# Kernel optimization log

Measured on AMD Instinct MI355X. Metric: run time of the kernel, lower is better.

## Reference

```python
import jax, jax.numpy as jnp
import numpy as np

N_NODES = 50000
IN, HID, OUT = 128, 128, 47
N_EDGES = 800000


def _glorot(key, shape):
    fan_in, fan_out = shape[1], shape[0]
    lim = np.sqrt(6.0 / (fan_in + fan_out)).astype(np.float32)
    return jax.random.uniform(key, shape, jnp.float32, -lim, lim)


def setup_inputs() -> dict:
    key = jax.random.key(0)
    ks = jax.random.split(key, 12)
    x = jax.random.normal(ks[0], (N_NODES, IN), jnp.float32)
    src = jax.random.randint(ks[1], (N_EDGES,), 0, N_NODES)
    dst = jax.random.randint(ks[2], (N_EDGES,), 0, N_NODES)
    return {
        "x": x, "src": src, "dst": dst,
        "w_self1": _glorot(ks[3], (HID, IN)),  "w_neigh1": _glorot(ks[4], (HID, IN)),  "b1": jnp.zeros((HID,), jnp.float32),
        "w_self2": _glorot(ks[5], (HID, HID)), "w_neigh2": _glorot(ks[6], (HID, HID)), "b2": jnp.zeros((HID,), jnp.float32),
        "w_self3": _glorot(ks[7], (OUT, HID)), "w_neigh3": _glorot(ks[8], (OUT, HID)), "b3": jnp.zeros((OUT,), jnp.float32),
    }


def _sage_conv(h, src, dst, w_self, w_neigh, b):
    # gather src features, mean-reduce per dst node (DGL copy_u + mean)
    msg = h[src]                                                  # [E, d]
    agg = jax.ops.segment_sum(msg, dst, num_segments=N_NODES)    # [N, d]
    deg = jax.ops.segment_sum(jnp.ones((dst.shape[0],), h.dtype), dst, num_segments=N_NODES)
    mean = agg / jnp.maximum(deg, 1.0)[:, None]
    # DGL SAGEConv('mean'): fc_self(h_dst) + fc_neigh(h_neigh); bias on fc_self only
    return h @ w_self.T + b + mean @ w_neigh.T


def reference(x, src, dst,
              w_self1, w_neigh1, b1,
              w_self2, w_neigh2, b2,
              w_self3, w_neigh3, b3):
    h = _sage_conv(x, src, dst, w_self1, w_neigh1, b1)
    h = jax.nn.relu(h)  # dropout is identity in eval mode
    h = _sage_conv(h, src, dst, w_self2, w_neigh2, b2)
    h = jax.nn.relu(h)
    h = _sage_conv(h, src, dst, w_self3, w_neigh3, b3)
    return h
```

## Files before the change

### kernel.cpp

```cpp
#include <hip/hip_runtime.h>

#define N_NODES 50000
#define N_EDGES 800000
#define DIM 128
#define OUTD 47
#define NBK 196
#define EPB 4096
#define NBIN ((N_EDGES + EPB - 1) / EPB)
#define XCVT_NB (N_NODES * DIM / 8 / 256)
#define WFNB 19

typedef __attribute__((ext_vector_type(8))) short v8s;
typedef __attribute__((ext_vector_type(8))) unsigned short v8u;
typedef __attribute__((ext_vector_type(4))) float v4f;
typedef __attribute__((ext_vector_type(2))) float v2f;

static __device__ __forceinline__ unsigned short f2bf(float f) {
    union { float f; unsigned int u; } v; v.f = f;
    unsigned int x = v.u;
    return (unsigned short)((x + 0x7fffu + ((x >> 16) & 1u)) >> 16);
}
static __device__ __forceinline__ unsigned char f2fp8(float f) {
    unsigned int pk = __builtin_amdgcn_cvt_pk_fp8_f32(f, f, 0, false);
    return (unsigned char)(pk & 0xffu);
}

__global__ __launch_bounds__(256) void k_prep(const float* __restrict__ x,
                                              unsigned short* __restrict__ xb,
                                              unsigned int* __restrict__ x8,
                                              const int* __restrict__ dst,
                                              int* __restrict__ parts,
                                              const float* __restrict__ ws1, const float* __restrict__ wn1,
                                              const float* __restrict__ ws2, const float* __restrict__ wn2,
                                              const float* __restrict__ ws3, const float* __restrict__ wn3,
                                              unsigned short* __restrict__ wf1,
                                              unsigned short* __restrict__ wf2,
                                              unsigned short* __restrict__ wf3) {
    __shared__ int hist[NBK];
    const int bx = blockIdx.x, tid = threadIdx.x;
    if (bx < XCVT_NB) {
        int i = bx * 256 + tid;
        float4 v0 = ((const float4*)x)[i * 2];
        float4 v1 = ((const float4*)x)[i * 2 + 1];
        ushort4 o0, o1;
        o0.x = f2bf(v0.x); o0.y = f2bf(v0.y); o0.z = f2bf(v0.z); o0.w = f2bf(v0.w);
        o1.x = f2bf(v1.x); o1.y = f2bf(v1.y); o1.z = f2bf(v1.z); o1.w = f2bf(v1.w);
        ((ushort4*)xb)[i * 2] = o0;
        ((ushort4*)xb)[i * 2 + 1] = o1;
        unsigned int a = __builtin_amdgcn_cvt_pk_fp8_f32(v0.x, v0.y, 0, false);
        a = __builtin_amdgcn_cvt_pk_fp8_f32(v0.z, v0.w, a, true);
        unsigned int b = __builtin_amdgcn_cvt_pk_fp8_f32(v1.x, v1.y, 0, false);
        b = __builtin_amdgcn_cvt_pk_fp8_f32(v1.z, v1.w, b, true);
        uint2 o; o.x = a; o.y = b;
        ((uint2*)x8)[i] = o;
    } else if (bx < XCVT_NB + NBIN) {
        const int j = bx - XCVT_NB;
        for (int i = tid; i < NBK; i += 256) hist[i] = 0;
        __syncthreads();
        const int e0 = j * EPB;
        const int ecnt = min(EPB, N_EDGES - e0);
        for (int r = tid; r < ecnt; r += 256)
            atomicAdd(&hist[dst[e0 + r] >> 8], 1);
        __syncthreads();
        for (int i = tid; i < NBK; i += 256) parts[j * NBK + i] = hist[i];
    } else {
        int b2 = bx - XCVT_NB - NBIN;
        const float *sw, *nw; unsigned short* ob; int t, J;
        if (b2 < 8)       { sw = ws1; nw = wn1; ob = wf1; t = b2;      J = DIM; }
        else if (b2 < 16) { sw = ws2; nw = wn2; ob = wf2; t = b2 - 8;  J = DIM; }
        else              { sw = ws3; nw = wn3; ob = wf3; t = b2 - 16; J = OUTD; }
        const int lane = tid & 63, cp = tid >> 6;
        const int j = t * 16 + (lane & 15);
        const int kb = (lane >> 4) * 8;
        #pragma unroll
        for (int c2 = 0; c2 < 2; ++c2) {
            int c = cp * 2 + c2;
            int k0 = c * 32 + kb;
            v8u o;
            #pragma unroll
            for (int i = 0; i < 8; ++i) {
                int k = k0 + i;
                float v = 0.f;
                if (j < J) v = (k < DIM) ? sw[j * DIM + k] : nw[j * DIM + (k - DIM)];
                o[i] = f2bf(v);
            }
            *(v8u*)(ob + ((size_t)((t * 8 + c) * 64 + lane)) * 8) = o;
        }
    }
}

__global__ __launch_bounds__(256) void k_bin(const int* __restrict__ src,
                                             const int* __restrict__ dst,
                                             const int* __restrict__ parts,
                                             unsigned int* __restrict__ packed) {
    __shared__ int s[256], gb[NBK], cnt[NBK];
    const int t = threadIdx.x;
    const int j = blockIdx.x;
    int ct = 0, cp = 0;
    for (int i = 0; i < NBIN; ++i) {
        int v = (t < NBK) ? parts[i * NBK + t] : 0;
        if (i == j) cp = ct;
        ct += v;
    }
    s[t] = ct;
    __syncthreads();
    for (int off = 1; off < 256; off <<= 1) {
        int u = (t >= off) ? s[t - off] : 0;
        __syncthreads();
        s[t] += u;
        __syncthreads();
    }
    if (t < NBK) { gb[t] = (s[t] - ct) + cp; cnt[t] = 0; }
    __syncthreads();
    const int e0 = j * EPB;
    const int ecnt = min(EPB, N_EDGES - e0);
    for (int r = t; r < ecnt; r += 256) {
        int sv = src[e0 + r], d = dst[e0 + r];
        int b = d >> 8;
        int loc = atomicAdd(&cnt[b], 1);
        packed[gb[b] + loc] = ((unsigned int)sv << 8) | (unsigned int)(d & 255);
    }
}

__global__ __launch_bounds__(256) void k_place(const unsigned int* __restrict__ packed,
                                               const int* __restrict__ parts,
                                               int* __restrict__ row_ptr,
                                               int* __restrict__ src_sorted) {
    __shared__ int s[256], baseL[NBK], totL[NBK];
    __shared__ int hist[256], cur[256];
    const int b = blockIdx.x, t = threadIdx.x;
    int ct = 0;
    for (int i = 0; i < NBIN; ++i)
        ct += (t < NBK) ? parts[i * NBK + t] : 0;
    s[t] = ct;
    hist[t] = 0;
    __syncthreads();
    for (int off = 1; off < 256; off <<= 1) {
        int u = (t >= off) ? s[t - off] : 0;
        __syncthreads();
        s[t] += u;
        __syncthreads();
    }
    if (t < NBK) { baseL[t] = s[t] - ct; totL[t] = ct; }
    __syncthreads();
    const int base = baseL[b], cb = totL[b];
    for (int i = t; i < cb; i += 256)
        atomicAdd(&hist[packed[base + i] & 255u], 1);
    __syncthreads();
    int v = hist[t];
    s[t] = v;
    __syncthreads();
    for (int off = 1; off < 256; off <<= 1) {
        int u = (t >= off) ? s[t - off] : 0;
        __syncthreads();
        s[t] += u;
        __syncthreads();
    }
    int excl = base + s[t] - v;
    int node = b * 256 + t;
    if (node < N_NODES) row_ptr[node] = excl;
    if (b == NBK - 1 && t == 255) row_ptr[N_NODES] = base + cb;
    cur[t] = excl;
    __syncthreads();
    for (int i = t; i < cb; i += 256) {
        unsigned int pkt = packed[base + i];
        int pos = atomicAdd(&cur[pkt & 255u], 1);
        src_sorted[pos] = (int)(pkt >> 8);
    }
}

static __device__ __forceinline__ void acc16(v2f* acc, uint4 u) {
    acc[0] += __builtin_amdgcn_cvt_pk_f32_fp8(u.x, false);
    acc[1] += __builtin_amdgcn_cvt_pk_f32_fp8(u.x, true);
    acc[2] += __builtin_amdgcn_cvt_pk_f32_fp8(u.y, false);
    acc[3] += __builtin_amdgcn_cvt_pk_f32_fp8(u.y, true);
    acc[4] += __builtin_amdgcn_cvt_pk_f32_fp8(u.z, false);
    acc[5] += __builtin_amdgcn_cvt_pk_f32_fp8(u.z, true);
    acc[6] += __builtin_amdgcn_cvt_pk_f32_fp8(u.w, false);
    acc[7] += __builtin_amdgcn_cvt_pk_f32_fp8(u.w, true);
}

template <int NT, bool RELU, bool OUTBF>
__global__ __launch_bounds__(256, 4) void k_layer(const unsigned short* __restrict__ Ab,
                                                  const unsigned char* __restrict__ g8,
                                                  const int* __restrict__ row_ptr,
                                                  const int* __restrict__ srcs,
                                                  const unsigned short* __restrict__ Wf,
                                                  const float* __restrict__ bias,
                                                  void* __restrict__ out,
                                                  unsigned char* __restrict__ out8,
                                                  int outdim) {
    __shared__ unsigned short Alds[64 * 256];
    const int tid = threadIdx.x;
    const int m0 = blockIdx.x * 64;
    #pragma unroll
    for (int i = 0; i < 4; ++i) {
        int t = tid + 256 * i;
        int row = t >> 4, ch = t & 15;
        int node = m0 + row; if (node >= N_NODES) node = N_NODES - 1;
        v8u v = *(const v8u*)(Ab + (size_t)node * DIM + ch * 8);
        *(v8u*)(Alds + row * 256 + ((ch * 8) ^ ((row & 7) * 8))) = v;
    }
    const int lane = tid & 63, wv = tid >> 6;
    const int gg = lane & 7;
    const int sub = (lane >> 3) & 1;
    const int ns = lane >> 4;
    for (int pass = 0; pass < 4; ++pass) {
        const int row = wv * 16 + pass * 4 + ns;
        const int n = m0 + row;
        int start = 0, end = 0;
        if (n < N_NODES) { start = row_ptr[n]; end = row_ptr[n + 1]; }
        v2f ga[8] = {};
        int e = start;
        int s0, s1, s2, s3;
        bool have = (e + 8 <= end);
        if (have) {
            s0 = srcs[e + sub]; s1 = srcs[e + 2 + sub];
            s2 = srcs[e + 4 + sub]; s3 = srcs[e + 6 + sub];
        }
        while (have) {
            uint4 u0 = *(const uint4*)(g8 + (size_t)s0 * DIM + gg * 16);
            uint4 u1 = *(const uint4*)(g8 + (size_t)s1 * DIM + gg * 16);
            uint4 u2 = *(const uint4*)(g8 + (size_t)s2 * DIM + gg * 16);
            uint4 u3 = *(const uint4*)(g8 + (size_t)s3 * DIM + gg * 16);
            e += 8;
            have = (e + 8 <= end);
            if (have) {
                s0 = srcs[e + sub]; s1 = srcs[e + 2 + sub];
                s2 = srcs[e + 4 + sub]; s3 = srcs[e + 6 + sub];
            }
            acc16(ga, u0); acc16(ga, u1); acc16(ga, u2); acc16(ga, u3);
        }
        if (e + 4 <= end) {
            int t0 = srcs[e + sub], t1 = srcs[e + 2 + sub];
            uint4 u0 = *(const uint4*)(g8 + (size_t)t0 * DIM + gg * 16);
            uint4 u1 = *(const uint4*)(g8 + (size_t)t1 * DIM + gg * 16);
            acc16(ga, u0); acc16(ga, u1);
            e += 4;
        }
        if (e + 2 <= end) {
            int t0 = srcs[e + sub];
            uint4 u0 = *(const uint4*)(g8 + (size_t)t0 * DIM + gg * 16);
            acc16(ga, u0);
            e += 2;
        }
        if (e < end && sub == 0) {
            int t0 = srcs[e];
            uint4 u0 = *(const uint4*)(g8 + (size_t)t0 * DIM + gg * 16);
            acc16(ga, u0);
        }
        #pragma unroll
        for (int i = 0; i < 8; ++i) {
            ga[i][0] += __shfl_xor(ga[i][0], 8);
            ga[i][1] += __shfl_xor(ga[i][1], 8);
        }
        int d = end - start;
        float inv = (d > 0) ? 1.f / (float)d : 0.f;
        v2f w0 = sub ? ga[4] : ga[0];
        v2f w1 = sub ? ga[5] : ga[1];
        v2f w2 = sub ? ga[6] : ga[2];
        v2f w3 = sub ? ga[7] : ga[3];
        v8u o;
        o[0] = f2bf(w0[0] * inv); o[1] = f2bf(w0[1] * inv);
        o[2] = f2bf(w1[0] * inv); o[3] = f2bf(w1[1] * inv);
        o[4] = f2bf(w2[0] * inv); o[5] = f2bf(w2[1] * inv);
        o[6] = f2bf(w3[0] * inv); o[7] = f2bf(w3[1] * inv);
        *(v8u*)(Alds + row * 256 + ((DIM + gg * 16 + sub * 8) ^ ((row & 7) * 8))) = o;
    }
    __syncthreads();
    const int m = lane & 15, qd = lane >> 4;
    const int arow = wv * 16 + m;
    v4f acc[NT] = {};
    #pragma unroll
    for (int c = 0; c < 8; ++c) {
        const int koff = c * 32 + qd * 8;
        v8s af = *(const v8s*)(Alds + arow * 256 + (koff ^ ((arow & 7) * 8)));
        #pragma unroll
        for (int t = 0; t < NT; ++t) {
            v8s wf = *(const v8s*)(Wf + ((size_t)((t * 8 + c) * 64 + lane)) * 8);
            acc[t] = __builtin_amdgcn_mfma_f32_16x16x32_bf16(af, wf, acc[t], 0, 0, 0);
        }
    }
    #pragma unroll
    for (int t = 0; t < NT; ++t) {
        int col = t * 16 + m;
        bool colok = (col < outdim);
        float bv = colok ? bias[col] : 0.f;
        #pragma unroll
        for (int r = 0; r < 4; ++r) {
            int nrow = m0 + wv * 16 + qd * 4 + r;
            if (colok && nrow < N_NODES) {
                float v = acc[t][r] + bv;
                if (RELU) v = fmaxf(v, 0.f);
                size_t idx = (size_t)nrow * outdim + col;
                if (OUTBF) {
                    ((unsigned short*)out)[idx] = f2bf(v);
                    out8[idx] = f2fp8(v);
                } else {
                    ((float*)out)[idx] = v;
                }
            }
        }
    }
}

extern "C" void kernel_launch(void* const* d_in, const int* in_sizes, int n_in,
                              void* d_out, int out_size, void* d_ws, size_t ws_size,
                              hipStream_t stream) {
    const float* x   = (const float*)d_in[0];
    const int*   src = (const int*)d_in[1];
    const int*   dst = (const int*)d_in[2];
    const float* ws1 = (const float*)d_in[3];
    const float* wn1 = (const float*)d_in[4];
    const float* b1  = (const float*)d_in[5];
    const float* ws2 = (const float*)d_in[6];
    const float* wn2 = (const float*)d_in[7];
    const float* b2  = (const float*)d_in[8];
    const float* ws3 = (const float*)d_in[9];
    const float* wn3 = (const float*)d_in[10];
    const float* b3  = (const float*)d_in[11];

    char* p = (char*)d_ws;
    auto alloc = [&](size_t bytes) { char* r = p; p += (bytes + 255) & ~(size_t)255; return r; };
    int*   row_ptr = (int*)alloc((size_t)(N_NODES + 1) * 4);
    int*   srcs    = (int*)alloc((size_t)N_EDGES * 4);
    unsigned int* packed = (unsigned int*)alloc((size_t)N_EDGES * 4);
    int*   parts   = (int*)alloc((size_t)NBIN * NBK * 4);
    unsigned short* xb  = (unsigned short*)alloc((size_t)N_NODES * DIM * 2);
    unsigned short* h1b = (unsigned short*)alloc((size_t)N_NODES * DIM * 2);
    unsigned short* h2b = (unsigned short*)alloc((size_t)N_NODES * DIM * 2);
    unsigned char*  h8a = (unsigned char*)alloc((size_t)N_NODES * DIM);
    unsigned char*  h8b = (unsigned char*)alloc((size_t)N_NODES * DIM);
    unsigned short* wf1 = (unsigned short*)alloc((size_t)8 * 8 * 64 * 8 * 2);
    unsigned short* wf2 = (unsigned short*)alloc((size_t)8 * 8 * 64 * 8 * 2);
    unsigned short* wf3 = (unsigned short*)alloc((size_t)3 * 8 * 64 * 8 * 2);

    k_prep<<<XCVT_NB + NBIN + WFNB, 256, 0, stream>>>(
        x, xb, (unsigned int*)h8a, dst, parts,
        ws1, wn1, ws2, wn2, ws3, wn3, wf1, wf2, wf3);
    k_bin<<<NBIN, 256, 0, stream>>>(src, dst, parts, packed);
    k_place<<<NBK, 256, 0, stream>>>(packed, parts, row_ptr, srcs);

    const int MB = (N_NODES + 63) / 64;

    k_layer<8, true, true><<<MB, 256, 0, stream>>>(xb,  h8a, row_ptr, srcs, wf1, b1, h1b, h8b, DIM);
    k_layer<8, true, true><<<MB, 256, 0, stream>>>(h1b, h8b, row_ptr, srcs, wf2, b2, h2b, h8a, DIM);
    k_layer<3, false, false><<<MB, 256, 0, stream>>>(h2b, h8a, row_ptr, srcs, wf3, b3, d_out, nullptr, OUTD);
}
```

Baseline: 238.3 us.

## Fuse CSR build and all three layers into persistent kernels with grid barriers

Result: slower. 577.0 us (+142.1%).

```diff
diff --git a/kernel.cpp b/kernel.cpp
--- a/kernel.cpp
+++ b/kernel.cpp
@@ -9,6 +9,7 @@
 #define NBIN ((N_EDGES + EPB - 1) / EPB)
 #define XCVT_NB (N_NODES * DIM / 8 / 256)
 #define WFNB 19
+#define NB_LAY ((N_NODES + 63) / 64)
 
 typedef __attribute__((ext_vector_type(8))) short v8s;
 typedef __attribute__((ext_vector_type(8))) unsigned short v8u;
@@ -23,6 +24,18 @@
 static __device__ __forceinline__ unsigned char f2fp8(float f) {
     unsigned int pk = __builtin_amdgcn_cvt_pk_fp8_f32(f, f, 0, false);
     return (unsigned char)(pk & 0xffu);
+}
+
+static __device__ __forceinline__ void gbar(int* bar, int nb) {
+    __syncthreads();
+    if (threadIdx.x == 0) {
+        __threadfence();
+        atomicAdd(bar, 1);
+        while (__hip_atomic_load(bar, __ATOMIC_ACQUIRE, __HIP_MEMORY_SCOPE_AGENT) < nb)
+            __builtin_amdgcn_s_sleep(2);
+        __threadfence();
+    }
+    __syncthreads();
 }
 
 __global__ __launch_bounds__(256) void k_prep(const float* __restrict__ x,
@@ -35,9 +48,11 @@
                                               const float* __restrict__ ws3, const float* __restrict__ wn3,
                                               unsigned short* __restrict__ wf1,
                                               unsigned short* __restrict__ wf2,
-                                              unsigned short* __restrict__ wf3) {
+                                              unsigned short* __restrict__ wf3,
+                                              int* __restrict__ bars) {
     __shared__ int hist[NBK];
     const int bx = blockIdx.x, tid = threadIdx.x;
+    if (bx == 0 && tid == 0) bars[0] = 0;
     if (bx < XCVT_NB) {
         int i = bx * 256 + tid;
         float4 v0 = ((const float4*)x)[i * 2];
@@ -89,13 +104,18 @@
     }
 }
 
-__global__ __launch_bounds__(256) void k_bin(const int* __restrict__ src,
+__global__ __launch_bounds__(256) void k_csr(const int* __restrict__ src,
                                              const int* __restrict__ dst,
                                              const int* __restrict__ parts,
-                                             unsigned int* __restrict__ packed) {
-    __shared__ int s[256], gb[NBK], cnt[NBK];
+                                             unsigned int* __restrict__ packed,
+                                             int* __restrict__ row_ptr,
+                                             int* __restrict__ src_sorted,
+                                             int* __restrict__ bars) {
+    __shared__ int s[256], gb[NBK], cnt[NBK], baseL[NBK], totL[NBK];
+    __shared__ int hist[256], cur[256];
     const int t = threadIdx.x;
     const int j = blockIdx.x;
+    if (j == 0 && t == 0) { bars[1] = 0; bars[2] = 0; }
     int ct = 0, cp = 0;
     for (int i = 0; i < NBIN; ++i) {
         int v = (t < NBK) ? parts[i * NBK + t] : 0;
@@ -110,30 +130,30 @@
         s[t] += u;
         __syncthreads();
     }
-    if (t < NBK) { gb[t] = (s[t] - ct) + cp; cnt[t] = 0; }
-    __syncthreads();
-    const int e0 = j * EPB;
-    const int ecnt = min(EPB, N_EDGES - e0);
-    for (int r = t; r < ecnt; r += 256) {
-        int sv = src[e0 + r], d = dst[e0 + r];
-        int b = d >> 8;
-        int loc = atomicAdd(&cnt[b], 1);
-        packed[gb[b] + loc] = ((unsigned int)sv << 8) | (unsigned int)(d & 255);
-    }
-}
-
-__global__ __launch_bounds__(256) void k_place(const unsigned int* __restrict__ packed,
-                                               const int* __restrict__ parts,
-                                               int* __restrict__ row_ptr,
-                                               int* __restrict__ src_sorted) {
-    __shared__ int s[256], baseL[NBK], totL[NBK];
-    __shared__ int hist[256], cur[256];
-    const int b = blockIdx.x, t = threadIdx.x;
-    int ct = 0;
-    for (int i = 0; i < NBIN; ++i)
-        ct += (t < NBK) ? parts[i * NBK + t] : 0;
-    s[t] = ct;
+    if (t < NBK) {
+        baseL[t] = s[t] - ct; totL[t] = ct;
+        gb[t] = (s[t] - ct) + cp; cnt[t] = 0;
+    }
+    __syncthreads();
+    {
+        const int e0 = j * EPB;
+        const int ecnt = min(EPB, N_EDGES - e0);
+        for (int r = t; r < ecnt; r += 256) {
+            int sv = src[e0 + r], d = dst[e0 + r];
+            int b = d >> 8;
+            int loc = atomicAdd(&cnt[b], 1);
+            packed[gb[b] + loc] = ((unsigned int)sv << 8) | (unsigned int)(d & 255);
+        }
+    }
+    gbar(&bars[0], NBIN);
+    const int base = baseL[j], cb = totL[j];
     hist[t] = 0;
+    __syncthreads();
+    for (int i = t; i < cb; i += 256)
+        atomicAdd(&hist[packed[base + i] & 255u], 1);
+    __syncthreads();
+    int v = hist[t];
+    s[t] = v;
     __syncthreads();
     for (int off = 1; off < 256; off <<= 1) {
         int u = (t >= off) ? s[t - off] : 0;
@@ -141,25 +161,10 @@
         s[t] += u;
         __syncthreads();
     }
-    if (t < NBK) { baseL[t] = s[t] - ct; totL[t] = ct; }
-    __syncthreads();
-    const int base = baseL[b], cb = totL[b];
-    for (int i = t; i < cb; i += 256)
-        atomicAdd(&hist[packed[base + i] & 255u], 1);
-    __syncthreads();
-    int v = hist[t];
-    s[t] = v;
-    __syncthreads();
-    for (int off = 1; off < 256; off <<= 1) {
-        int u = (t >= off) ? s[t - off] : 0;
-        __syncthreads();
-        s[t] += u;
-        __syncthreads();
-    }
     int excl = base + s[t] - v;
-    int node = b * 256 + t;
+    int node = j * 256 + t;
     if (node < N_NODES) row_ptr[node] = excl;
-    if (b == NBK - 1 && t == 255) row_ptr[N_NODES] = base + cb;
+    if (j == NBK - 1 && t == 255) row_ptr[N_NODES] = base + cb;
     cur[t] = excl;
     __syncthreads();
     for (int i = t; i < cb; i += 256) {
@@ -180,27 +185,17 @@
     acc[7] += __builtin_amdgcn_cvt_pk_f32_fp8(u.w, true);
 }
 
-template <int NT, bool RELU, bool OUTBF>
-__global__ __launch_bounds__(256, 4) void k_layer(const unsigned short* __restrict__ Ab,
-                                                  const unsigned char* __restrict__ g8,
-                                                  const int* __restrict__ row_ptr,
-                                                  const int* __restrict__ srcs,
-                                                  const unsigned short* __restrict__ Wf,
-                                                  const float* __restrict__ bias,
-                                                  void* __restrict__ out,
-                                                  unsigned char* __restrict__ out8,
-                                                  int outdim) {
-    __shared__ unsigned short Alds[64 * 256];
+template <int NT, bool RELU, bool FINAL>
+static __device__ __forceinline__ void layer_phase(unsigned short* Alds, int m0,
+                                                   const unsigned char* __restrict__ g8,
+                                                   const int* __restrict__ row_ptr,
+                                                   const int* __restrict__ srcs,
+                                                   const unsigned short* __restrict__ Wf,
+                                                   const float* __restrict__ bias,
+                                                   float* __restrict__ outf,
+                                                   unsigned char* __restrict__ out8,
+                                                   int outdim) {
     const int tid = threadIdx.x;
-    const int m0 = blockIdx.x * 64;
-    #pragma unroll
-    for (int i = 0; i < 4; ++i) {
-        int t = tid + 256 * i;
-        int row = t >> 4, ch = t & 15;
-        int node = m0 + row; if (node >= N_NODES) node = N_NODES - 1;
-        v8u v = *(const v8u*)(Ab + (size_t)node * DIM + ch * 8);
-        *(v8u*)(Alds + row * 256 + ((ch * 8) ^ ((row & 7) * 8))) = v;
-    }
     const int lane = tid & 63, wv = tid >> 6;
     const int gg = lane & 7;
     const int sub = (lane >> 3) & 1;
@@ -281,6 +276,7 @@
             acc[t] = __builtin_amdgcn_mfma_f32_16x16x32_bf16(af, wf, acc[t], 0, 0, 0);
         }
     }
+    __syncthreads();
     #pragma unroll
     for (int t = 0; t < NT; ++t) {
         int col = t * 16 + m;
@@ -288,20 +284,52 @@
         float bv = colok ? bias[col] : 0.f;
         #pragma unroll
         for (int r = 0; r < 4; ++r) {
-            int nrow = m0 + wv * 16 + qd * 4 + r;
+            int lrow = wv * 16 + qd * 4 + r;
+            int nrow = m0 + lrow;
             if (colok && nrow < N_NODES) {
                 float v = acc[t][r] + bv;
                 if (RELU) v = fmaxf(v, 0.f);
-                size_t idx = (size_t)nrow * outdim + col;
-                if (OUTBF) {
-                    ((unsigned short*)out)[idx] = f2bf(v);
-                    out8[idx] = f2fp8(v);
+                if (FINAL) {
+                    outf[(size_t)nrow * outdim + col] = v;
                 } else {
-                    ((float*)out)[idx] = v;
+                    out8[(size_t)nrow * DIM + col] = f2fp8(v);
+                    int gsh = (col & 0x78);
+                    Alds[lrow * 256 + (gsh ^ ((lrow & 7) * 8)) + (col & 7)] = f2bf(v);
                 }
             }
         }
     }
+}
+
+__global__ __launch_bounds__(256, 4) void k_layers(const unsigned short* __restrict__ xb,
+                                                   unsigned char* __restrict__ h8a,
+                                                   unsigned char* __restrict__ h8b,
+                                                   const int* __restrict__ row_ptr,
+                                                   const int* __restrict__ srcs,
+                                                   const unsigned short* __restrict__ wf1,
+                                                   const unsigned short* __restrict__ wf2,
+                                                   const unsigned short* __restrict__ wf3,
+                                                   const float* __restrict__ b1,
+                                                   const float* __restrict__ b2,
+                                                   const float* __restrict__ b3,
+                                                   float* __restrict__ d_out,
+                                                   int* __restrict__ bars) {
+    __shared__ unsigned short Alds[64 * 256];
+    const int tid = threadIdx.x;
+    const int m0 = blockIdx.x * 64;
+    #pragma unroll
+    for (int i = 0; i < 4; ++i) {
+        int t = tid + 256 * i;
+        int row = t >> 4, ch = t & 15;
+        int node = m0 + row; if (node >= N_NODES) node = N_NODES - 1;
+        v8u v = *(const v8u*)(xb + (size_t)node * DIM + ch * 8);
+        *(v8u*)(Alds + row * 256 + ((ch * 8) ^ ((row & 7) * 8))) = v;
+    }
+    layer_phase<8, true, false>(Alds, m0, h8a, row_ptr, srcs, wf1, b1, nullptr, h8b, DIM);
+    gbar(&bars[1], NB_LAY);
+    layer_phase<8, true, false>(Alds, m0, h8b, row_ptr, srcs, wf2, b2, nullptr, h8a, DIM);
+    gbar(&bars[2], NB_LAY);
+    layer_phase<3, false, true>(Alds, m0, h8a, row_ptr, srcs, wf3, b3, d_out, nullptr, OUTD);
 }
 
 extern "C" void kernel_launch(void* const* d_in, const int* in_sizes, int n_in,
@@ -327,23 +355,18 @@
     unsigned int* packed = (unsigned int*)alloc((size_t)N_EDGES * 4);
     int*   parts   = (int*)alloc((size_t)NBIN * NBK * 4);
     unsigned short* xb  = (unsigned short*)alloc((size_t)N_NODES * DIM * 2);
-    unsigned short* h1b = (unsigned short*)alloc((size_t)N_NODES * DIM * 2);
-    unsigned short* h2b = (unsigned short*)alloc((size_t)N_NODES * DIM * 2);
     unsigned char*  h8a = (unsigned char*)alloc((size_t)N_NODES * DIM);
     unsigned char*  h8b = (unsigned char*)alloc((size_t)N_NODES * DIM);
     unsigned short* wf1 = (unsigned short*)alloc((size_t)8 * 8 * 64 * 8 * 2);
     unsigned short* wf2 = (unsigned short*)alloc((size_t)8 * 8 * 64 * 8 * 2);
     unsigned short* wf3 = (unsigned short*)alloc((size_t)3 * 8 * 64 * 8 * 2);
+    int*   bars = (int*)alloc(256);
 
     k_prep<<<XCVT_NB + NBIN + WFNB, 256, 0, stream>>>(
         x, xb, (unsigned int*)h8a, dst, parts,
-        ws1, wn1, ws2, wn2, ws3, wn3, wf1, wf2, wf3);
-    k_bin<<<NBIN, 256, 0, stream>>>(src, dst, parts, packed);
-    k_place<<<NBK, 256, 0, stream>>>(packed, parts, row_ptr, srcs);
-
-    const int MB = (N_NODES + 63) / 64;
-
-    k_layer<8, true, true><<<MB, 256, 0, stream>>>(xb,  h8a, row_ptr, srcs, wf1, b1, h1b, h8b, DIM);
-    k_layer<8, true, true><<<MB, 256, 0, stream>>>(h1b, h8b, row_ptr, srcs, wf2, b2, h2b, h8a, DIM);
-    k_layer<3, false, false><<<MB, 256, 0, stream>>>(h2b, h8a, row_ptr, srcs, wf3, b3, d_out, nullptr, OUTD);
-}
+        ws1, wn1, ws2, wn2, ws3, wn3, wf1, wf2, wf3, bars);
+    k_csr<<<NBIN, 256, 0, stream>>>(src, dst, parts, packed, row_ptr, srcs, bars);
+    k_layers<<<NB_LAY, 256, 0, stream>>>(xb, h8a, h8b, row_ptr, srcs,
+                                         wf1, wf2, wf3, b1, b2, b3,
+                                         (float*)d_out, bars);
+}
```
